# Performance work log

Hardware: AMD Instinct MI355X
Metric: run time of the kernel (lower is better)

The kernel has to match this reference:

```python
import jax, jax.numpy as jnp
import numpy as np

B, N, D = 8, 65536, 3
K = 64                 # num_centers
NPOINT = 4096
M = NPOINT // K * 2    # max_neighbors = 128
S = NPOINT // K        # fps samples per group = 64
NITER = 10             # KMeans default Niter


def _sqdist(src, dst):
    # ||s||^2 + ||d||^2 - 2 s.d   (same math as (s-d)^2 sum, GEMM form)
    s2 = (src ** 2).sum(-1)[:, :, None]          # [B,N,1]
    d2 = (dst ** 2).sum(-1)[:, None, :]          # [B,1,K]
    return s2 + d2 - 2.0 * jnp.einsum('bnd,bkd->bnk', src, dst)


def _kmeans(x):
    Bb, Nn, Dd = x.shape
    c = x[:, :K, :]
    bidx = jnp.arange(Bb)[:, None]               # broadcast with cl [B,N]
    for _ in range(NITER):
        cl = jnp.argmin(_sqdist(x, c), axis=2)   # [B,N] cluster codes
        c = jnp.zeros((Bb, K, Dd), x.dtype).at[bidx, cl].add(x)
        ncl = jnp.zeros((Bb, K), x.dtype).at[bidx, cl].add(1.0)
        c = c / ncl[:, :, None]
    return c


def _query_neighbor(x, centers):
    dist = _sqdist(x, centers)                   # [B,N,K]
    negd = -jnp.transpose(dist, (0, 2, 1))       # [B,K,N]
    _, nidx = jax.lax.top_k(negd, M)             # M nearest points per center
    bidx = jnp.arange(x.shape[0])[:, None, None]
    return x[bidx, nidx]                         # [B,K,M,3]


def _batch_fps(xyz, farthest0):
    # xyz: [B,G,Nn,3]; sequential farthest-point sampling per group
    Bb, G, Nn, _ = xyz.shape
    dist0 = jnp.full((Bb, G, Nn), 1e10, xyz.dtype)

    def step(carry, _):
        distance, farthest = carry
        centroid = jnp.take_along_axis(xyz, farthest[:, :, None, None], axis=2)  # [B,G,1,3]
        d = ((xyz - centroid) ** 2).sum(-1)       # [B,G,Nn]
        distance = jnp.minimum(distance, d)
        new_far = jnp.argmax(distance, -1).astype(farthest.dtype)
        return (distance, new_far), farthest      # store index BEFORE update

    _, idx = jax.lax.scan(step, (dist0, farthest0), None, length=S)
    idx = jnp.transpose(idx, (1, 2, 0))           # [B,G,S]
    idx3 = jnp.broadcast_to(idx[..., None], idx.shape + (3,))
    new_xyz = jnp.take_along_axis(xyz, idx3, axis=2)  # [B,G,S,3]
    return new_xyz.reshape(Bb, G * S, 3)


def setup_inputs() -> dict:
    key = jax.random.key(0)
    k1, k2 = jax.random.split(key)
    x = jax.random.normal(k1, (B, N, D), dtype=jnp.float32)
    farthest0 = jax.random.randint(k2, (B, K), 0, M, dtype=jnp.int32)
    return {"x": x, "farthest0": farthest0}


def reference(x, farthest0):
    centers = _kmeans(x)                  # [B,K,3]
    neighbor = _query_neighbor(x, centers)  # [B,K,M,3]
    new_xyz = _batch_fps(neighbor, farthest0)  # [B, NPOINT, 3]
    return new_xyz, centers
```

## Files before the change

### kernel.cpp

```cpp
#include <hip/hip_runtime.h>
#include <stdint.h>

#pragma clang fp contract(off)

#define B 8
#define N 65536
#define KC 64
#define M 128
#define S 64
#define NITER 10
#define NWAVES 16
#define HPAD 257
#define SAMPLE 8192
#define SCAP 2048
#define CAPG 3072
#define WCAP 512
#define CSTRIDE 32
#define UPD_T 1024
#define RANGE 16384
#define NRANGE (N / RANGE)
#define PPT (RANGE / UPD_T)
#define GBATCH 2048

using u32 = unsigned int;
using u64 = unsigned long long;

__device__ __forceinline__ float sq3(float a, float b, float c) {
  return __fadd_rn(__fadd_rn(__fmul_rn(a, a), __fmul_rn(b, b)), __fmul_rn(c, c));
}
__device__ __forceinline__ float dot3(float x0, float x1, float x2,
                                      float c0, float c1, float c2) {
  return __fadd_rn(__fadd_rn(__fmul_rn(x0, c0), __fmul_rn(x1, c1)), __fmul_rn(x2, c2));
}
__device__ __forceinline__ float distf(float s2, float d2, float dt) {
  return __fsub_rn(__fadd_rn(s2, d2), __fmul_rn(2.0f, dt));
}
__device__ __forceinline__ u32 fkey(float f) {
  u32 u = __float_as_uint(f);
  return (u & 0x80000000u) ? ~u : (u | 0x80000000u);
}


__global__ void k_init_centers(const float* __restrict__ x, float* __restrict__ centers) {
  int i = blockIdx.x * blockDim.x + threadIdx.x;
  if (i >= B * KC * 3) return;
  int b = i / (KC * 3);
  int r = i % (KC * 3);
  centers[i] = x[(size_t)b * N * 3 + r];
}

__global__ __launch_bounds__(256)
void k_assign(const float* __restrict__ x, const float* __restrict__ centers,
              unsigned char* __restrict__ cl) {
  __shared__ float4 cs[KC];
  int g = blockIdx.x;
  int b = g & 7;
  int chunk = g >> 3;
  int t = threadIdx.x;
  if (t < KC) {
    float a0 = centers[(b * KC + t) * 3 + 0];
    float a1 = centers[(b * KC + t) * 3 + 1];
    float a2 = centers[(b * KC + t) * 3 + 2];
    cs[t] = make_float4(a0, a1, a2, sq3(a0, a1, a2));
  }
  __syncthreads();
  int q = chunk * 256 + t;
  const float4* xb4 = (const float4*)(x + (size_t)b * N * 3);
  float4 A = xb4[3 * q], Bv = xb4[3 * q + 1], C = xb4[3 * q + 2];
  float p0x = A.x, p0y = A.y, p0z = A.z;
  float p1x = A.w, p1y = Bv.x, p1z = Bv.y;
  float p2x = Bv.z, p2y = Bv.w, p2z = C.x;
  float p3x = C.y, p3y = C.z, p3z = C.w;
  float s0 = sq3(p0x, p0y, p0z);
  float s1 = sq3(p1x, p1y, p1z);
  float s2 = sq3(p2x, p2y, p2z);
  float s3 = sq3(p3x, p3y, p3z);
  float inf = __int_as_float(0x7f800000);
  float b0 = inf, b1 = inf, b2 = inf, b3 = inf;
  int i0 = 0, i1 = 0, i2 = 0, i3 = 0;
  for (int k = 0; k < KC; ++k) {
    float4 cc = cs[k];
    float d0 = distf(s0, cc.w, dot3(p0x, p0y, p0z, cc.x, cc.y, cc.z));
    float d1 = distf(s1, cc.w, dot3(p1x, p1y, p1z, cc.x, cc.y, cc.z));
    float d2 = distf(s2, cc.w, dot3(p2x, p2y, p2z, cc.x, cc.y, cc.z));
    float d3 = distf(s3, cc.w, dot3(p3x, p3y, p3z, cc.x, cc.y, cc.z));
    if (d0 < b0) { b0 = d0; i0 = k; }
    if (d1 < b1) { b1 = d1; i1 = k; }
    if (d2 < b2) { b2 = d2; i2 = k; }
    if (d3 < b3) { b3 = d3; i3 = k; }
  }
  *(u32*)(cl + (size_t)b * N + 4 * q) =
      (u32)i0 | ((u32)i1 << 8) | ((u32)i2 << 16) | ((u32)i3 << 24);
}

__global__ __launch_bounds__(UPD_T)
void k_cluster_update(const float* __restrict__ x, const unsigned char* __restrict__ cl,
                      float* __restrict__ centers) {
  __shared__ unsigned short midx[RANGE];
  __shared__ float bcoord[3][GBATCH + 1];
  __shared__ int woff[NWAVES];
  __shared__ int sCnt;
  int g = blockIdx.x;
  int bk = ((g & 7) << 6) | (g >> 3);
  int b = bk >> 6, k = bk & 63;
  int t = threadIdx.x, lane = t & 63, wid = t >> 6;
  const unsigned char* clb = cl + (size_t)b * N;
  const float* xb = x + (size_t)b * N * 3;
  float acc = 0.f;
  int cntAll = 0;

  for (int r = 0; r < NRANGE; ++r) {
    const uint4* cp = (const uint4*)(clb + r * RANGE);
    uint4 v = cp[t];
    u32 wsv[4] = {v.x, v.y, v.z, v.w};
    int m = 0;
#pragma unroll
    for (int j = 0; j < PPT; ++j)
      m += (((wsv[j >> 2] >> ((j & 3) * 8)) & 255u) == (u32)k);
    int incl = m;
#pragma unroll
    for (int o = 1; o < 64; o <<= 1) {
      int u = __shfl_up(incl, o);
      if (lane >= o) incl += u;
    }
    if (lane == 63) woff[wid] = incl;
    __syncthreads();
    if (t == 0) {
      int run = 0;
      for (int w = 0; w < NWAVES; ++w) { int vv = woff[w]; woff[w] = run; run += vv; }
      sCnt = run;
    }
    __syncthreads();
    int off = woff[wid] + incl - m;
    int mcnt = sCnt;
    int base = t * PPT;
#pragma unroll
    for (int j = 0; j < PPT; ++j) {
      if (((wsv[j >> 2] >> ((j & 3) * 8)) & 255u) == (u32)k)
        midx[off++] = (unsigned short)(base + j);
    }
    __syncthreads();
    for (int bo = 0; bo < mcnt; bo += GBATCH) {
      int bn = min(GBATCH, mcnt - bo);
      for (int i = t; i < bn; i += UPD_T) {
        int li = midx[bo + i];
        size_t src = ((size_t)(r * RANGE + li)) * 3;
        bcoord[0][i] = xb[src];
        bcoord[1][i] = xb[src + 1];
        bcoord[2][i] = xb[src + 2];
      }
      __syncthreads();
      if (wid == 0 && lane < 3) {
        const float* mb = &bcoord[lane][0];
#pragma unroll 8
        for (int i = 0; i < bn; ++i) acc = __fadd_rn(acc, mb[i]);
      }
      __syncthreads();
    }
    cntAll += mcnt;
    __syncthreads();
  }
  if (wid == 0 && lane < 3)
    centers[bk * 3 + lane] = __fdiv_rn(acc, (float)cntAll);
}

__global__ __launch_bounds__(256)
void k_thresh(const float* __restrict__ x, const float* __restrict__ centers,
              u32* __restrict__ thr, u32* __restrict__ cnt) {
  __shared__ u32 whist[4 * HPAD];
  __shared__ int sv[256];
  __shared__ u32 skeys[SCAP];
  __shared__ float4 scen;
  __shared__ u32 sSel;
  __shared__ int sNeed, sCntBin, sNum;
  int g = blockIdx.x;
  int bk = ((g & 7) << 6) | (g >> 3);
  int b = bk >> 6;
  int t = threadIdx.x, wid = t >> 6;
  if (t == 0) {
    float c0 = centers[bk * 3], c1 = centers[bk * 3 + 1], c2 = centers[bk * 3 + 2];
    scen = make_float4(c0, c1, c2, sq3(c0, c1, c2));
    cnt[bk * CSTRIDE] = 0;
    sNum = 0;
  }
  for (int i = t; i < 4 * HPAD; i += 256) whist[i] = 0;
  __syncthreads();
  float c0 = scen.x, c1 = scen.y, c2 = scen.z, d2 = scen.w;
  const float2* xb2 = (const float2*)(x + (size_t)b * N * 3);

  for (int p = t; p < SAMPLE / 2; p += 256) {
    float2 A = xb2[3 * p], Bv = xb2[3 * p + 1], C = xb2[3 * p + 2];
    float d0 = distf(sq3(A.x, A.y, Bv.x), d2, dot3(A.x, A.y, Bv.x, c0, c1, c2));
    float d1 = distf(sq3(Bv.y, C.x, C.y), d2, dot3(Bv.y, C.x, C.y, c0, c1, c2));
    atomicAdd(&whist[wid * HPAD + (fkey(d0) >> 24)], 1u);
    atomicAdd(&whist[wid * HPAD + (fkey(d1) >> 24)], 1u);
  }
  __syncthreads();
  int own = (int)(whist[0 * HPAD + t] + whist[1 * HPAD + t] +
                  whist[2 * HPAD + t] + whist[3 * HPAD + t]);
  sv[t] = own;
  __syncthreads();
  for (int off = 1; off < 256; off <<= 1) {
    int add = (t >= off) ? sv[t - off] : 0;
    __syncthreads();
    sv[t] += add;
    __syncthreads();
  }
  if (sv[t] >= M && sv[t] - own < M) {
    sSel = (u32)t; sNeed = M - (sv[t] - own); sCntBin = own;
  }
  __syncthreads();
  u32 selByte = sSel;
  int need = sNeed;
  int cntBin = sCntBin;
  u32 prefix = selByte << 24;

  if (cntBin <= SCAP) {
    for (int p = t; p < SAMPLE / 2; p += 256) {
      float2 A = xb2[3 * p], Bv = xb2[3 * p + 1], C = xb2[3 * p + 2];
      float d0 = distf(sq3(A.x, A.y, Bv.x), d2, dot3(A.x, A.y, Bv.x, c0, c1, c2));
      float d1 = distf(sq3(Bv.y, C.x, C.y), d2, dot3(Bv.y, C.x, C.y, c0, c1, c2));
      u32 k0 = fkey(d0), k1 = fkey(d1);
      if ((k0 >> 24) == selByte) skeys[atomicAdd(&sNum, 1)] = k0;
      if ((k1 >> 24) == selByte) skeys[atomicAdd(&sNum, 1)] = k1;
    }
    __syncthreads();
    int ne = sNum;
    for (int sh = 16; sh >= 0; sh -= 8) {
      whist[t] = 0;
      __syncthreads();
      for (int i = t; i < ne; i += 256) {
        u32 kk = skeys[i];
        if ((kk >> (sh + 8)) == (prefix >> (sh + 8)))
          atomicAdd(&whist[(kk >> sh) & 255u], 1u);
      }
      __syncthreads();
      int own2 = (int)whist[t];
      sv[t] = own2;
      __syncthreads();
      for (int off = 1; off < 256; off <<= 1) {
        int add = (t >= off) ? sv[t - off] : 0;
        __syncthreads();
        sv[t] += add;
        __syncthreads();
      }
      if (sv[t] >= need && sv[t] - own2 < need) {
        sSel = prefix | ((u32)t << sh);
        sNeed = need - (sv[t] - own2);
      }
      __syncthreads();
      prefix = sSel; need = sNeed;
      __syncthreads();
    }
    if (t == 0) thr[bk] = prefix;
  } else {
    if (t == 0) thr[bk] = prefix | 0x00FFFFFFu;
  }
}

__global__ __launch_bounds__(256)
void k_scatter_test(const float* __restrict__ x, const float* __restrict__ centers,
                    const u32* __restrict__ thr, u32* __restrict__ cnt,
                    u32* __restrict__ cand) {
  __shared__ float4 cs[KC];
  __shared__ u32 lthr[KC];
  __shared__ u64 wm0[4][KC], wm1[4][KC];
  __shared__ u32 wbase[4][KC];
  int g = blockIdx.x;
  int b = g & 7;
  int chunk = g >> 3;
  int t = threadIdx.x, lane = t & 63, wid = t >> 6;
  if (t < KC) {
    float a0 = centers[(b * KC + t) * 3 + 0];
    float a1 = centers[(b * KC + t) * 3 + 1];
    float a2 = centers[(b * KC + t) * 3 + 2];
    cs[t] = make_float4(a0, a1, a2, sq3(a0, a1, a2));
    lthr[t] = thr[b * KC + t];
  }
  __syncthreads();
  int pr = chunk * 256 + t;
  const float2* xb2 = (const float2*)(x + (size_t)b * N * 3);
  float2 A = xb2[3 * pr], Bv = xb2[3 * pr + 1], C = xb2[3 * pr + 2];
  float s20 = sq3(A.x, A.y, Bv.x);
  float s21 = sq3(Bv.y, C.x, C.y);
  u32 n0 = 2 * pr, n1 = 2 * pr + 1;
  u64 ltm = ((u64)1 << lane) - 1;

  for (int k = 0; k < KC; ++k) {
    float4 cc = cs[k];
    float d0 = distf(s20, cc.w, dot3(A.x, A.y, Bv.x, cc.x, cc.y, cc.z));
    float d1 = distf(s21, cc.w, dot3(Bv.y, C.x, C.y, cc.x, cc.y, cc.z));
    u64 m0 = __ballot(fkey(d0) <= lthr[k]);
    u64 m1 = __ballot(fkey(d1) <= lthr[k]);
    if (lane == 0) { wm0[wid][k] = m0; wm1[wid][k] = m1; }
  }
  __syncthreads();
  if (t < KC) {
    u32 pc[4];
    u32 total = 0;
#pragma unroll
    for (int w = 0; w < 4; ++w) {
      pc[w] = (u32)(__popcll(wm0[w][t]) + __popcll(wm1[w][t]));
      total += pc[w];
    }
    u32 base = (total > 0) ? atomicAdd(&cnt[(b * KC + t) * CSTRIDE], total) : 0u;
#pragma unroll
    for (int w = 0; w < 4; ++w) { wbase[w][t] = base; base += pc[w]; }
  }
  __syncthreads();
  u64 mybit = (u64)1 << lane;
  for (int k = 0; k < KC; ++k) {
    u64 m0 = wm0[wid][k], m1 = wm1[wid][k];
    if ((m0 | m1) == 0) continue;
    u32 wb = wbase[wid][k];
    u32* cb = cand + (size_t)(b * KC + k) * CAPG;
    if (m0 & mybit) {
      u32 pos = wb + (u32)__popcll(m0 & ltm);
      if (pos < CAPG) cb[pos] = n0;
    }
    if (m1 & mybit) {
      u32 pos = wb + (u32)__popcll(m0) + (u32)__popcll(m1 & ltm);
      if (pos < CAPG) cb[pos] = n1;
    }
  }
}

__global__ __launch_bounds__(256)
void k_topk_sort(const float* __restrict__ x, const float* __restrict__ centers,
                 const u32* __restrict__ cnt, const u32* __restrict__ cand,
                 float* __restrict__ neighbor) {
  __shared__ u64 candList[CAPG];
  __shared__ u32 hist[256];
  __shared__ u64 wbuf[WCAP];
  __shared__ u64 lessList[M];
  __shared__ u32 eqList[256];
  __shared__ u32 sSel;
  __shared__ int sNeed;
  __shared__ int cntW, cntLess, cntEq;
  __shared__ float4 scen;
  int g = blockIdx.x;
  int bk = ((g & 7) << 6) | (g >> 3);
  int b = bk >> 6;
  int t = threadIdx.x, lane = t & 63, wid = t >> 6;
  if (t == 0) {
    float c0 = centers[bk * 3], c1 = centers[bk * 3 + 1], c2 = centers[bk * 3 + 2];
    scen = make_float4(c0, c1, c2, sq3(c0, c1, c2));
    cntW = 0;
  }
  __syncthreads();
  float c0 = scen.x, c1 = scen.y, c2 = scen.z, d2 = scen.w;
  const float* xb = x + (size_t)b * N * 3;
  int cc = (int)cnt[bk * CSTRIDE];

  if (cc <= CAPG) {
    const u32* cb = cand + (size_t)bk * CAPG;
    for (int i = t; i < cc; i += 256) {
      u32 n = cb[i];
      float x0 = xb[n * 3], x1 = xb[n * 3 + 1], x2 = xb[n * 3 + 2];
      float d = distf(sq3(x0, x1, x2), d2, dot3(x0, x1, x2, c0, c1, c2));
      candList[i] = ((u64)fkey(d) << 32) | n;
    }
    __syncthreads();
    u32 prefix = 0;
    int need = M;
    for (int r = 3; r >= 0; --r) {
      int sh = r * 8;
      hist[t] = 0;
      __syncthreads();
      for (int i = t; i < cc; i += 256) {
        u32 key = (u32)(candList[i] >> 32);
        bool ok = (r == 3) || ((key >> (sh + 8)) == (prefix >> (sh + 8)));
        if (ok) atomicAdd(&hist[(key >> sh) & 255u], 1u);
      }
      __syncthreads();
      if (wid == 0) {
        u32 h0 = hist[4 * lane + 0], h1 = hist[4 * lane + 1];
        u32 h2 = hist[4 * lane + 2], h3 = hist[4 * lane + 3];
        u32 lsum = h0 + h1 + h2 + h3;
        u32 incl = lsum;
#pragma unroll
        for (int o = 1; o < 64; o <<= 1) {
          u32 u = __shfl_up(incl, o);
          if (lane >= o) incl += u;
        }
        u32 excl = incl - lsum;
        if ((int)excl < need && need <= (int)incl) {
          u32 hh[4] = {h0, h1, h2, h3};
          u32 cum = excl; int bin = -1; u32 bc = 0;
#pragma unroll
          for (int j = 0; j < 4; ++j) {
            if (bin < 0 && (int)(cum + hh[j]) >= need) { bin = 4 * lane + j; bc = cum; }
            cum += hh[j];
          }
          sSel = prefix | ((u32)bin << sh);
          sNeed = need - (int)bc;
        }
      }
      __syncthreads();
      prefix = sSel; need = sNeed;
      __syncthreads();
    }
    u32 K128 = prefix;
    for (int i = t; i < cc; i += 256) {
      u64 e = candList[i];
      if ((u32)(e >> 32) <= K128) {
        int p = atomicAdd(&cntW, 1);
        if (p < WCAP) wbuf[p] = e;
      }
    }
    __syncthreads();
    int wcnt = cntW;
    if (wcnt <= WCAP) {
      for (int i = t; i < WCAP; i += 256) if (i >= wcnt) wbuf[i] = ~0ull;
      __syncthreads();
      for (int ksz = 2; ksz <= WCAP; ksz <<= 1) {
        for (int j = ksz >> 1; j > 0; j >>= 1) {
          for (int idx = t; idx < WCAP; idx += 256) {
            int ixj = idx ^ j;
            if (ixj > idx) {
              u64 a = wbuf[idx], bb = wbuf[ixj];
              bool up = ((idx & ksz) == 0);
              if (up ? (a > bb) : (a < bb)) { wbuf[idx] = bb; wbuf[ixj] = a; }
            }
          }
          __syncthreads();
        }
      }
      if (t < M) {
        int idx = (int)(wbuf[t] & 0xFFFFFFFFu);
        size_t src = ((size_t)b * N + idx) * 3;
        size_t dst = ((size_t)bk * M + t) * 3;
        neighbor[dst]     = x[src];
        neighbor[dst + 1] = x[src + 1];
        neighbor[dst + 2] = x[src + 2];
      }
      return;
    }
  }

  if (t == 0) { cntLess = 0; cntEq = 0; }
  __syncthreads();
  u32 prefix = 0;
  int need = M;
  for (int r = 3; r >= 0; --r) {
    for (int i = t; i < 256; i += 256) hist[i] = 0;
    __syncthreads();
    int sh = r * 8;
    for (int n = t; n < N; n += 256) {
      float x0 = xb[n * 3], x1 = xb[n * 3 + 1], x2 = xb[n * 3 + 2];
      float d = distf(sq3(x0, x1, x2), d2, dot3(x0, x1, x2, c0, c1, c2));
      u32 key = fkey(d);
      bool ok = (r == 3) || ((key >> (sh + 8)) == (prefix >> (sh + 8)));
      if (ok) atomicAdd(&hist[(key >> sh) & 255u], 1u);
    }
    __syncthreads();
    if (t == 0) {
      int cum = 0;
      for (int bin = 0; bin < 256; ++bin) {
        int c = (int)hist[bin];
        if (cum + c >= need) { sSel = prefix | ((u32)bin << sh); sNeed = need - cum; break; }
        cum += c;
      }
    }
    __syncthreads();
    prefix = sSel; need = sNeed;
    __syncthreads();
  }
  u32 K128 = prefix;

  for (int n = t; n < N; n += 256) {
    float x0 = xb[n * 3], x1 = xb[n * 3 + 1], x2 = xb[n * 3 + 2];
    float d = distf(sq3(x0, x1, x2), d2, dot3(x0, x1, x2, c0, c1, c2));
    u32 key = fkey(d);
    if (key < K128) {
      int p = atomicAdd(&cntLess, 1);
      if (p < M) lessList[p] = ((u64)key << 32) | (u32)n;
    } else if (key == K128) {
      int p = atomicAdd(&cntEq, 1);
      if (p < 256) eqList[p] = (u32)n;
    }
  }
  __syncthreads();
  int nl = cntLess;
  int ne2 = cntEq;
  for (int i = t; i < M; i += 256) if (i >= nl) lessList[i] = ~0ull;
  for (int i = t; i < 256; i += 256) if (i >= ne2) eqList[i] = 0xFFFFFFFFu;
  __syncthreads();

  for (int ksz = 2; ksz <= M; ksz <<= 1) {
    for (int j = ksz >> 1; j > 0; j >>= 1) {
      for (int idx = t; idx < M; idx += 256) {
        int ixj = idx ^ j;
        if (ixj > idx) {
          u64 a = lessList[idx], bb = lessList[ixj];
          bool up = ((idx & ksz) == 0);
          if (up ? (a > bb) : (a < bb)) { lessList[idx] = bb; lessList[ixj] = a; }
        }
      }
      __syncthreads();
    }
  }
  for (int ksz = 2; ksz <= 256; ksz <<= 1) {
    for (int j = ksz >> 1; j > 0; j >>= 1) {
      for (int idx = t; idx < 256; idx += 256) {
        int ixj = idx ^ j;
        if (ixj > idx) {
          u32 a = eqList[idx], bb = eqList[ixj];
          bool up = ((idx & ksz) == 0);
          if (up ? (a > bb) : (a < bb)) { eqList[idx] = bb; eqList[ixj] = a; }
        }
      }
      __syncthreads();
    }
  }

  if (t < M) {
    int idx = (t < nl) ? (int)(lessList[t] & 0xFFFFFFFFu) : (int)eqList[t - nl];
    size_t src = ((size_t)b * N + idx) * 3;
    size_t dst = ((size_t)bk * M + t) * 3;
    neighbor[dst]     = x[src];
    neighbor[dst + 1] = x[src + 1];
    neighbor[dst + 2] = x[src + 2];
  }
}

__global__ __launch_bounds__(64)
void k_fps(const float* __restrict__ neighbor, const int* __restrict__ farthest0,
           const float* __restrict__ centers, float* __restrict__ out) {
  __shared__ float4 pts[M];
  int bg = blockIdx.x;
  int b = bg >> 6, g = bg & 63;
  int t = threadIdx.x;
  {
    int i = bg * 64 + t;
    if (i < B * KC * 3) out[B * 4096 * 3 + i] = centers[i];
  }
  const float* nb = neighbor + (size_t)bg * M * 3;
  float ax = nb[6 * t],     ay = nb[6 * t + 1], az = nb[6 * t + 2];
  float bx = nb[6 * t + 3], by = nb[6 * t + 4], bz = nb[6 * t + 5];
  pts[2 * t]     = make_float4(ax, ay, az, 0.f);
  pts[2 * t + 1] = make_float4(bx, by, bz, 0.f);
  int far = farthest0[bg];
  float dist0 = 1e10f, dist1 = 1e10f;
  __syncthreads();
  float* ob = out + ((size_t)b * 4096 + g * 64) * 3;
  for (int s = 0; s < S; ++s) {
    if ((far >> 1) == t) {
      if (far & 1) { ob[3 * s] = bx; ob[3 * s + 1] = by; ob[3 * s + 2] = bz; }
      else         { ob[3 * s] = ax; ob[3 * s + 1] = ay; ob[3 * s + 2] = az; }
    }
    float4 cc = pts[far];
    float d0 = sq3(__fsub_rn(ax, cc.x), __fsub_rn(ay, cc.y), __fsub_rn(az, cc.z));
    float d1 = sq3(__fsub_rn(bx, cc.x), __fsub_rn(by, cc.y), __fsub_rn(bz, cc.z));
    dist0 = fminf(dist0, d0);
    dist1 = fminf(dist1, d1);
    u64 k0 = ((u64)__float_as_uint(dist0) << 32) | (u32)(M - 1 - 2 * t);
    u64 k1 = ((u64)__float_as_uint(dist1) << 32) | (u32)(M - 2 - 2 * t);
    u64 key = (k0 > k1) ? k0 : k1;
#pragma unroll
    for (int off = 1; off < 64; off <<= 1) {
      u64 o = __shfl_xor(key, off);
      if (o > key) key = o;
    }
    far = M - 1 - (int)(key & 0xFFFFFFFFu);
  }
}

extern "C" void kernel_launch(void* const* d_in, const int* in_sizes, int n_in,
                              void* d_out, int out_size, void* d_ws, size_t ws_size,
                              hipStream_t stream) {
  const float* x = (const float*)d_in[0];
  const int* farthest0 = (const int*)d_in[1];
  float* out = (float*)d_out;

  char* w = (char*)d_ws;
  float* centers         = (float*)(w);
  unsigned char* cl      = (unsigned char*)(w + 8192);
  u32* thr               = (u32*)(w + 8192 + 524288);
  u32* cnt               = (u32*)(w + 8192 + 524288 + 4096);
  float* neighbor        = (float*)(w + 8192 + 524288 + 4096 + 65536);
  u32* cand              = (u32*)(w + 8192 + 524288 + 4096 + 65536 + 786432);

  k_init_centers<<<6, 256, 0, stream>>>(x, centers);
  for (int it = 0; it < NITER; ++it) {
    k_assign<<<B * 64, 256, 0, stream>>>(x, centers, cl);
    k_cluster_update<<<B * KC, UPD_T, 0, stream>>>(x, cl, centers);
  }
  k_thresh<<<B * KC, 256, 0, stream>>>(x, centers, thr, cnt);
  k_scatter_test<<<B * 128, 256, 0, stream>>>(x, centers, thr, cnt, cand);
  k_topk_sort<<<B * KC, 256, 0, stream>>>(x, centers, cnt, cand, neighbor);
  k_fps<<<B * KC, M / 2, 0, stream>>>(neighbor, farthest0, centers, out);
}
```

Measured before the change: 483.1 us.

## Shrink cluster update to 256 threads and double-buffer coordinate gathers behind summation

Rewrites the k_cluster_update kernel to use 256 threads, each scanning 64 cluster codes. The per-wave prefix combine no longer needs a serial thread-0 pass or an extra barrier. Coordinate gathering now goes through a double-buffered shared-memory batch, so waves 1-3 load the next batch while three threads of wave 0 serially add up the current one. This is meant to hide gather latency behind the serial sequential-order float summation and to cut barriers, at the cost of fewer loader threads per block. Other edits only rename variables.

```diff
diff --git a/kernel.cpp b/kernel.cpp
--- a/kernel.cpp
+++ b/kernel.cpp
@@ -9,21 +9,21 @@
 #define M 128
 #define S 64
 #define NITER 10
-#define NWAVES 16
 #define HPAD 257
 #define SAMPLE 8192
 #define SCAP 2048
 #define CAPG 3072
 #define WCAP 512
 #define CSTRIDE 32
-#define UPD_T 1024
-#define RANGE 16384
-#define NRANGE (N / RANGE)
-#define PPT (RANGE / UPD_T)
-#define GBATCH 2048
+#define NCHK 64
+#define URANGE 16384
+#define UNR (N / URANGE)
+#define UPPT 64
+#define UBATCH 1024
 
 using u32 = unsigned int;
 using u64 = unsigned long long;
+using u16 = unsigned short;
 
 __device__ __forceinline__ float sq3(float a, float b, float c) {
   return __fadd_rn(__fadd_rn(__fmul_rn(a, a), __fmul_rn(b, b)), __fmul_rn(c, c));
@@ -93,13 +93,12 @@
       (u32)i0 | ((u32)i1 << 8) | ((u32)i2 << 16) | ((u32)i3 << 24);
 }
 
-__global__ __launch_bounds__(UPD_T)
+__global__ __launch_bounds__(256)
 void k_cluster_update(const float* __restrict__ x, const unsigned char* __restrict__ cl,
                       float* __restrict__ centers) {
-  __shared__ unsigned short midx[RANGE];
-  __shared__ float bcoord[3][GBATCH + 1];
-  __shared__ int woff[NWAVES];
-  __shared__ int sCnt;
+  __shared__ u16 midx[URANGE];
+  __shared__ float bcoord[2][3][UBATCH + 1];
+  __shared__ int woff[4];
   int g = blockIdx.x;
   int bk = ((g & 7) << 6) | (g >> 3);
   int b = bk >> 6, k = bk & 63;
@@ -109,14 +108,24 @@
   float acc = 0.f;
   int cntAll = 0;
 
-  for (int r = 0; r < NRANGE; ++r) {
-    const uint4* cp = (const uint4*)(clb + r * RANGE);
-    uint4 v = cp[t];
-    u32 wsv[4] = {v.x, v.y, v.z, v.w};
+  for (int r = 0; r < UNR; ++r) {
+    u32 words[16];
+    {
+      const uint4* cp = (const uint4*)(clb + (size_t)r * URANGE) + t * 4;
+#pragma unroll
+      for (int j = 0; j < 4; ++j) {
+        uint4 v = cp[j];
+        words[4 * j] = v.x; words[4 * j + 1] = v.y;
+        words[4 * j + 2] = v.z; words[4 * j + 3] = v.w;
+      }
+    }
     int m = 0;
 #pragma unroll
-    for (int j = 0; j < PPT; ++j)
-      m += (((wsv[j >> 2] >> ((j & 3) * 8)) & 255u) == (u32)k);
+    for (int j = 0; j < 16; ++j) {
+      u32 w4 = words[j];
+      m += (int)((w4 & 255u) == (u32)k) + (int)(((w4 >> 8) & 255u) == (u32)k)
+         + (int)(((w4 >> 16) & 255u) == (u32)k) + (int)(((w4 >> 24) & 255u) == (u32)k);
+    }
     int incl = m;
 #pragma unroll
     for (int o = 1; o < 64; o <<= 1) {
@@ -125,43 +134,55 @@
     }
     if (lane == 63) woff[wid] = incl;
     __syncthreads();
-    if (t == 0) {
-      int run = 0;
-      for (int w = 0; w < NWAVES; ++w) { int vv = woff[w]; woff[w] = run; run += vv; }
-      sCnt = run;
-    }
-    __syncthreads();
-    int off = woff[wid] + incl - m;
-    int mcnt = sCnt;
-    int base = t * PPT;
-#pragma unroll
-    for (int j = 0; j < PPT; ++j) {
-      if (((wsv[j >> 2] >> ((j & 3) * 8)) & 255u) == (u32)k)
-        midx[off++] = (unsigned short)(base + j);
-    }
-    __syncthreads();
-    for (int bo = 0; bo < mcnt; bo += GBATCH) {
-      int bn = min(GBATCH, mcnt - bo);
-      for (int i = t; i < bn; i += UPD_T) {
-        int li = midx[bo + i];
-        size_t src = ((size_t)(r * RANGE + li)) * 3;
-        bcoord[0][i] = xb[src];
-        bcoord[1][i] = xb[src + 1];
-        bcoord[2][i] = xb[src + 2];
-      }
-      __syncthreads();
-      if (wid == 0 && lane < 3) {
-        const float* mb = &bcoord[lane][0];
+    int w0 = woff[0], w1 = woff[1], w2v = woff[2], w3 = woff[3];
+    int tot = w0 + w1 + w2v + w3;
+    int wbase = (wid > 0 ? w0 : 0) + (wid > 1 ? w1 : 0) + (wid > 2 ? w2v : 0);
+    int off = wbase + incl - m;
+    int base = t * UPPT;
+#pragma unroll
+    for (int j = 0; j < 16; ++j) {
+      u32 w4 = words[j];
+#pragma unroll
+      for (int s = 0; s < 4; ++s)
+        if (((w4 >> (8 * s)) & 255u) == (u32)k) midx[off++] = (u16)(base + 4 * j + s);
+    }
+    __syncthreads();
+    int rbase = r * URANGE;
+    int nb = (tot + UBATCH - 1) / UBATCH;
+    if (t >= 64 && nb > 0) {
+      int bn = min(UBATCH, tot);
+      for (int i = t - 64; i < bn; i += 192) {
+        int li = rbase + (int)midx[i];
+        bcoord[0][0][i] = xb[3 * li];
+        bcoord[0][1][i] = xb[3 * li + 1];
+        bcoord[0][2][i] = xb[3 * li + 2];
+      }
+    }
+    __syncthreads();
+    for (int z = 0; z < nb; ++z) {
+      if (t >= 64) {
+        if (z + 1 < nb) {
+          int bo = (z + 1) * UBATCH;
+          int bn = min(UBATCH, tot - bo);
+          int pb = (z + 1) & 1;
+          for (int i = t - 64; i < bn; i += 192) {
+            int li = rbase + (int)midx[bo + i];
+            bcoord[pb][0][i] = xb[3 * li];
+            bcoord[pb][1][i] = xb[3 * li + 1];
+            bcoord[pb][2][i] = xb[3 * li + 2];
+          }
+        }
+      } else if (t < 3) {
+        const float* bb = &bcoord[z & 1][t][0];
+        int bn = min(UBATCH, tot - z * UBATCH);
 #pragma unroll 8
-        for (int i = 0; i < bn; ++i) acc = __fadd_rn(acc, mb[i]);
-      }
-      __syncthreads();
-    }
-    cntAll += mcnt;
-    __syncthreads();
-  }
-  if (wid == 0 && lane < 3)
-    centers[bk * 3 + lane] = __fdiv_rn(acc, (float)cntAll);
+        for (int i = 0; i < bn; ++i) acc = __fadd_rn(acc, bb[i]);
+      }
+      __syncthreads();
+    }
+    cntAll += tot;
+  }
+  if (t < 3) centers[bk * 3 + t] = __fdiv_rn(acc, (float)cntAll);
 }
 
 __global__ __launch_bounds__(256)
@@ -230,9 +251,9 @@
       whist[t] = 0;
       __syncthreads();
       for (int i = t; i < ne; i += 256) {
-        u32 kk = skeys[i];
-        if ((kk >> (sh + 8)) == (prefix >> (sh + 8)))
-          atomicAdd(&whist[(kk >> sh) & 255u], 1u);
+        u32 kkk = skeys[i];
+        if ((kkk >> (sh + 8)) == (prefix >> (sh + 8)))
+          atomicAdd(&whist[(kkk >> sh) & 255u], 1u);
       }
       __syncthreads();
       int own2 = (int)whist[t];
@@ -409,9 +430,9 @@
       }
     }
     __syncthreads();
-    int wcnt = cntW;
-    if (wcnt <= WCAP) {
-      for (int i = t; i < WCAP; i += 256) if (i >= wcnt) wbuf[i] = ~0ull;
+    int wcnt2 = cntW;
+    if (wcnt2 <= WCAP) {
+      for (int i = t; i < WCAP; i += 256) if (i >= wcnt2) wbuf[i] = ~0ull;
       __syncthreads();
       for (int ksz = 2; ksz <= WCAP; ksz <<= 1) {
         for (int j = ksz >> 1; j > 0; j >>= 1) {
@@ -457,9 +478,9 @@
     if (t == 0) {
       int cum = 0;
       for (int bin = 0; bin < 256; ++bin) {
-        int c = (int)hist[bin];
-        if (cum + c >= need) { sSel = prefix | ((u32)bin << sh); sNeed = need - cum; break; }
-        cum += c;
+        int ccv = (int)hist[bin];
+        if (cum + ccv >= need) { sSel = prefix | ((u32)bin << sh); sNeed = need - cum; break; }
+        cum += ccv;
       }
     }
     __syncthreads();
@@ -574,20 +595,20 @@
   float* out = (float*)d_out;
 
   char* w = (char*)d_ws;
-  float* centers         = (float*)(w);
-  unsigned char* cl      = (unsigned char*)(w + 8192);
-  u32* thr               = (u32*)(w + 8192 + 524288);
-  u32* cnt               = (u32*)(w + 8192 + 524288 + 4096);
-  float* neighbor        = (float*)(w + 8192 + 524288 + 4096 + 65536);
-  u32* cand              = (u32*)(w + 8192 + 524288 + 4096 + 65536 + 786432);
+  float* centers  = (float*)(w);
+  unsigned char* cl = (unsigned char*)(w + 8192);
+  u32* thr        = (u32*)(w + 8192 + 524288);
+  u32* cnt        = (u32*)(w + 8192 + 524288 + 4096);
+  float* neighbor = (float*)(w + 8192 + 524288 + 4096 + 65536);
+  u32* cand       = (u32*)(w + 8192 + 524288 + 4096 + 65536 + 786432);
 
   k_init_centers<<<6, 256, 0, stream>>>(x, centers);
   for (int it = 0; it < NITER; ++it) {
-    k_assign<<<B * 64, 256, 0, stream>>>(x, centers, cl);
-    k_cluster_update<<<B * KC, UPD_T, 0, stream>>>(x, cl, centers);
+    k_assign<<<B * NCHK, 256, 0, stream>>>(x, centers, cl);
+    k_cluster_update<<<B * KC, 256, 0, stream>>>(x, cl, centers);
   }
   k_thresh<<<B * KC, 256, 0, stream>>>(x, centers, thr, cnt);
-  k_scatter_test<<<B * 128, 256, 0, stream>>>(x, centers, thr, cnt, cand);
+  k_scatter_test<<<B * NCHK * 2, 256, 0, stream>>>(x, centers, thr, cnt, cand);
   k_topk_sort<<<B * KC, 256, 0, stream>>>(x, centers, cnt, cand, neighbor);
   k_fps<<<B * KC, M / 2, 0, stream>>>(neighbor, farthest0, centers, out);
 }
```

Result: slower. 519.8 us (+7.6%).
